# Kernel optimization log

Hardware: AMD Instinct MI355X
Metric: run time of the kernel (lower is better)

## Reference

```python
import jax, jax.numpy as jnp
import numpy as np

TIME_STEPS = 50
LEFT_PAD = 250 // TIME_STEPS            # 5
MAX_DELAY = LEFT_PAD if LEFT_PAD % 2 == 1 else LEFT_PAD + 1  # 5 (odd)
SIG = float(MAX_DELAY // 2)             # 2.0, frozen
CIN = 34 * 34 * 2                       # 2312
HID = 300
NOUT = 10
BETA = 0.9
THRESH = 1.0
BATCH = 128


def setup_inputs() -> dict:
    key = jax.random.key(0)
    k = jax.random.split(key, 6)
    data = jax.random.normal(k[0], (BATCH, TIME_STEPS, CIN), jnp.float32)
    W1 = jax.random.normal(k[1], (HID, CIN), jnp.float32) / np.sqrt(CIN * MAX_DELAY).astype(np.float32)
    P1 = jax.random.uniform(k[2], (HID, CIN), jnp.float32, -SIG, SIG)
    b1 = jnp.zeros((HID,), jnp.float32)
    W2 = jax.random.normal(k[3], (NOUT, HID), jnp.float32) / np.sqrt(HID * MAX_DELAY).astype(np.float32)
    P2 = jax.random.uniform(k[4], (NOUT, HID), jnp.float32, -SIG, SIG)
    b2 = jnp.zeros((NOUT,), jnp.float32)
    return {"data": data, "W1": W1, "P1": P1, "b1": b1, "W2": W2, "P2": P2, "b2": b2}


def make_gauss_kernel(W, P):
    # DCLS 'gauss': weight W placed at learnable position P (centered at KS//2)
    # with Gaussian of width SIG, normalized over the KS taps. kernel_count=1.
    idx = jnp.arange(MAX_DELAY, dtype=W.dtype)              # [KS]
    c = P[..., None] + (MAX_DELAY // 2)                     # [O, I, 1]
    g = jnp.exp(-0.5 * ((idx - c) / SIG) ** 2)              # [O, I, KS]
    g = g / (g.sum(-1, keepdims=True) + 1e-7)
    return W[..., None] * g                                 # [O, I, KS]


def delay_conv(x, W, P, b):
    # x: [B, Cin, L], valid conv with synthesized kernel -> [B, Cout, L-KS+1]
    K = make_gauss_kernel(W, P)
    y = jax.lax.conv_general_dilated(x, K, window_strides=(1,), padding='VALID',
                                     dimension_numbers=('NCH', 'OIH', 'NCH'))
    return y + b[None, :, None]


def lif_scan(x):
    # snntorch Leaky (reset-by-subtraction, reset detached):
    #   mem_t = beta*mem_{t-1} + x_t - H(mem_{t-1}-thr)*thr ;  spk_t = H(mem_t-thr)
    # x: [B, C, T] -> (spk [T,B,C], mem [T,B,C])
    def step(mem, xt):
        reset = (mem > THRESH).astype(xt.dtype)
        mem_new = BETA * mem + xt - reset * THRESH
        spk = (mem_new > THRESH).astype(xt.dtype)
        return mem_new, (spk, mem_new)

    xs = jnp.moveaxis(x, 2, 0)                              # [T, B, C]
    mem0 = jnp.zeros(x.shape[:2], x.dtype)
    _, (spks, mems) = jax.lax.scan(step, mem0, xs)
    return spks, mems


def reference(data, W1, P1, b1, W2, P2, b2):
    # pad time (dim -2) on the left, permute to [B, Cin, T+pad]
    x = jnp.pad(data, ((0, 0), (LEFT_PAD, 0), (0, 0)))
    x = jnp.transpose(x, (0, 2, 1))                         # [B, CIN, T+pad]
    x = delay_conv(x, W1, P1, b1)                           # [B, HID, T1]
    spk1, _ = lif_scan(x)                                   # [T1, B, HID]
    h = jnp.moveaxis(spk1, 0, 2)                            # [B, HID, T1]
    h = jnp.pad(h, ((0, 0), (0, 0), (LEFT_PAD, 0)))
    y = delay_conv(h, W2, P2, b2)                           # [B, NOUT, T2]
    spk2, mem2 = lif_scan(y)                                # [T2, B, NOUT] each
    return spk2, mem2
```

## Files before the change

### kernel.cpp

```cpp
#include <hip/hip_runtime.h>

#define BSZ  128
#define TT   50
#define CIN  2312
#define HID  300
#define NOUT 10
#define KS   5
#define T1   51
#define T2   52

#define NC32 73
#define KFRAG_U 20480

typedef unsigned int u32;
typedef unsigned short u16;
typedef __attribute__((ext_vector_type(8))) short s16x8;
typedef __attribute__((ext_vector_type(4))) float f32x4;

#define EK1f 0.88249690258459546f
#define EK2f 0.60653065971263342f
#define EK3f 0.32465246735834974f
#define EK4f 0.13533528323661270f

static __device__ __forceinline__ u16 bfhi(float x) {
  u32 u = __float_as_uint(x);
  return (u16)((u + 0x7fffu + ((u >> 16) & 1u)) >> 16);
}
static __device__ __forceinline__ float bf2f(u16 h) {
  return __uint_as_float(((u32)h) << 16);
}

__global__ __launch_bounds__(256) void snn_prepm(
    const float* __restrict__ W1, const float* __restrict__ P1,
    u16* __restrict__ K1bf)
{
  const int c  = blockIdx.x;
  const int ow = blockIdx.y;
  const int tid = threadIdx.x;
  const int nt = tid >> 6, ll = tid & 63;
  const int g = ll >> 4, lr = ll & 15;
  const int o  = ow * 64 + nt * 16 + lr;
  const int ib = c * 32 + g * 8;

  s16x8 hv[5], lv[5];
#pragma unroll
  for (int k = 0; k < 5; ++k)
#pragma unroll
    for (int j = 0; j < 8; ++j) { hv[k][j] = 0; lv[k][j] = 0; }

  if (o < HID) {
    const float* wrow = W1 + (size_t)o * CIN;
    const float* prow = P1 + (size_t)o * CIN;
#pragma unroll
    for (int j = 0; j < 8; ++j) {
      const int i = ib + j;
      if (i < CIN) {
        const float w1 = wrow[i], p1 = prow[i];
        const float cc = p1 + 2.0f;
        const float E0 = __expf(-0.125f * cc * cc);
        const float U  = __expf(0.25f * cc);
        const float u2 = U * U;
        const float e0 = E0;
        const float e1 = E0 * U * EK1f;
        const float e2 = E0 * u2 * EK2f;
        const float e3 = E0 * (u2 * U) * EK3f;
        const float e4 = E0 * (u2 * u2) * EK4f;
        const float inv = 1.0f / (((((e0 + e1) + e2) + e3) + e4) + 1e-7f);
        const float vk[5] = { w1 * (e0 * inv), w1 * (e1 * inv),
                              w1 * (e2 * inv), w1 * (e3 * inv),
                              w1 * (e4 * inv) };
#pragma unroll
        for (int k = 0; k < 5; ++k) {
          const u16 h = bfhi(vk[k]);
          const u16 lo = bfhi(vk[k] - bf2f(h));
          hv[k][j] = (short)h; lv[k][j] = (short)lo;
        }
      }
    }
  }
  u16* base = K1bf + ((size_t)ow * NC32 + c) * KFRAG_U + nt * 1024 + ll * 8;
#pragma unroll
  for (int k = 0; k < 5; ++k) {
    *(s16x8*)(base + k * 4096)       = hv[k];
    *(s16x8*)(base + k * 4096 + 512) = lv[k];
  }
}

__global__ __launch_bounds__(256, 2) void snn_l1s(
    const float* __restrict__ data, const u16* __restrict__ K1bf,
    float* __restrict__ pbuf)
{
  __shared__ __align__(16) double dsm[2720];
  u16* A16 = (u16*)dsm;

  const int tid = threadIdx.x;
  const int bid = blockIdx.x;
  const int g  = bid & 7;
  const int r  = bid >> 3;
  const int s  = r & 1;
  const int u  = r >> 1;
  const int x  = g * 80 + u;
  const int ow = x >> 7;
  const int b  = x & 127;

  const int c_lo = s ? 37 : 0;
  const int c_hi = s ? 73 : 37;

  const int w  = tid >> 6, l = tid & 63;
  const int lr = l & 15, lg = l >> 4;
  const int wr = w >> 1, wc = w & 1;
  const int abase_u = (32 * wr + lr) * 40 + lg * 8;

  const float* dbase = data + (size_t)b * (TT * CIN);
  const u16* kbn = K1bf + (size_t)ow * NC32 * KFRAG_U + l * 8;
  const int ntg0 = wc * 2, ntg1 = wc * 2 + 1;

  const int s1 = tid >> 2;
  const int j4 = tid & 3;
  const int tp = s1 - 5;
  const bool avld = (tp >= 0) && (tp < TT);
  const float* aptr = dbase + (size_t)(avld ? tp : 0) * CIN + j4 * 8;

  if (tid < 80) {
    s16x8 z;
#pragma unroll
    for (int j = 0; j < 8; ++j) z[j] = 0;
    const int rr = tid / 20, off = (tid % 20) * 8;
    *(s16x8*)(A16 + rr * 2720 + 2560 + off) = z;
  }

#define LOADA(CC)                                                             \
  {                                                                           \
    const bool iv_ = avld && (((CC) < 72) || (j4 == 0));                      \
    const float* pp_ = aptr + (size_t)(CC) * 32;                              \
    ra0 = iv_ ? *(const float4*)(pp_)     : make_float4(0.f, 0.f, 0.f, 0.f);  \
    ra1 = iv_ ? *(const float4*)(pp_ + 4) : make_float4(0.f, 0.f, 0.f, 0.f);  \
  }

#define STAGE_A(CC)                                                           \
  {                                                                           \
    const float f_[8] = { ra0.x, ra0.y, ra0.z, ra0.w,                         \
                          ra1.x, ra1.y, ra1.z, ra1.w };                       \
    s16x8 hv_, lv_;                                                           \
    _Pragma("unroll")                                                         \
    for (int j = 0; j < 8; ++j) {                                             \
      const u16 h_ = bfhi(f_[j]);                                             \
      hv_[j] = (short)h_;                                                     \
      lv_[j] = (short)bfhi(f_[j] - bf2f(h_));                                 \
    }                                                                         \
    u16* bn_ = A16 + ((CC) & 1) * 5440;                                       \
    const int woff_ = s1 * 40 + j4 * 8;                                       \
    *(s16x8*)(bn_ + woff_) = hv_;                                             \
    *(s16x8*)(bn_ + 2720 + woff_) = lv_;                                      \
  }

  s16x8 bh[5][2], bl[5][2];
#pragma unroll
  for (int k = 0; k < 5; ++k) {
    const u16* cb_ = kbn + (size_t)c_lo * KFRAG_U + k * 4096;
    bh[k][0] = *(const s16x8*)(cb_ + ntg0 * 1024);
    bh[k][1] = *(const s16x8*)(cb_ + ntg1 * 1024);
    bl[k][0] = *(const s16x8*)(cb_ + ntg0 * 1024 + 512);
    bl[k][1] = *(const s16x8*)(cb_ + ntg1 * 1024 + 512);
  }

  f32x4 accf[2][2];
  double accd[2][2][4];
#pragma unroll
  for (int m = 0; m < 2; ++m)
#pragma unroll
    for (int n = 0; n < 2; ++n)
#pragma unroll
      for (int q = 0; q < 4; ++q) { accf[m][n][q] = 0.f; accd[m][n][q] = 0.0; }

  float4 ra0, ra1;
  LOADA(c_lo);
  STAGE_A(c_lo);
  LOADA(c_lo + 1);
  __syncthreads();

  for (int c = c_lo; c < c_hi; ++c) {
    if (c + 1 < c_hi) {
      STAGE_A(c + 1);
      if (c + 2 < c_hi) LOADA(c + 2);
    }

    {
      const u16* bc_ = A16 + (c & 1) * 5440;
      const int rc = c + 1;
#pragma unroll
      for (int k = 0; k < 5; ++k) {
        const s16x8 ah0 = *(const s16x8*)(bc_ + abase_u + k * 40);
        const s16x8 al0 = *(const s16x8*)(bc_ + 2720 + abase_u + k * 40);
        const s16x8 ah1 = *(const s16x8*)(bc_ + abase_u + (16 + k) * 40);
        const s16x8 al1 = *(const s16x8*)(bc_ + 2720 + abase_u + (16 + k) * 40);

        accf[0][0] = __builtin_amdgcn_mfma_f32_16x16x32_bf16(ah0, bh[k][0], accf[0][0], 0, 0, 0);
        accf[0][0] = __builtin_amdgcn_mfma_f32_16x16x32_bf16(al0, bh[k][0], accf[0][0], 0, 0, 0);
        accf[0][0] = __builtin_amdgcn_mfma_f32_16x16x32_bf16(ah0, bl[k][0], accf[0][0], 0, 0, 0);

        accf[0][1] = __builtin_amdgcn_mfma_f32_16x16x32_bf16(ah0, bh[k][1], accf[0][1], 0, 0, 0);
        accf[0][1] = __builtin_amdgcn_mfma_f32_16x16x32_bf16(al0, bh[k][1], accf[0][1], 0, 0, 0);
        accf[0][1] = __builtin_amdgcn_mfma_f32_16x16x32_bf16(ah0, bl[k][1], accf[0][1], 0, 0, 0);

        accf[1][0] = __builtin_amdgcn_mfma_f32_16x16x32_bf16(ah1, bh[k][0], accf[1][0], 0, 0, 0);
        accf[1][0] = __builtin_amdgcn_mfma_f32_16x16x32_bf16(al1, bh[k][0], accf[1][0], 0, 0, 0);
        accf[1][0] = __builtin_amdgcn_mfma_f32_16x16x32_bf16(ah1, bl[k][0], accf[1][0], 0, 0, 0);

        accf[1][1] = __builtin_amdgcn_mfma_f32_16x16x32_bf16(ah1, bh[k][1], accf[1][1], 0, 0, 0);
        accf[1][1] = __builtin_amdgcn_mfma_f32_16x16x32_bf16(al1, bh[k][1], accf[1][1], 0, 0, 0);
        accf[1][1] = __builtin_amdgcn_mfma_f32_16x16x32_bf16(ah1, bl[k][1], accf[1][1], 0, 0, 0);

        if (rc < c_hi) {
          const u16* cb_ = kbn + (size_t)rc * KFRAG_U + k * 4096;
          bh[k][0] = *(const s16x8*)(cb_ + ntg0 * 1024);
          bh[k][1] = *(const s16x8*)(cb_ + ntg1 * 1024);
          bl[k][0] = *(const s16x8*)(cb_ + ntg0 * 1024 + 512);
          bl[k][1] = *(const s16x8*)(cb_ + ntg1 * 1024 + 512);
        }
      }
    }

#pragma unroll
    for (int m = 0; m < 2; ++m)
#pragma unroll
      for (int n = 0; n < 2; ++n)
#pragma unroll
        for (int q = 0; q < 4; ++q) {
          accd[m][n][q] += (double)accf[m][n][q];
          accf[m][n][q] = 0.f;
        }
    __syncthreads();
  }
#undef LOADA
#undef STAGE_A

  float* pb = pbuf + (((size_t)s * 5 + ow) * 128 + b) * 3264;
#pragma unroll
  for (int m = 0; m < 2; ++m)
#pragma unroll
    for (int n = 0; n < 2; ++n)
#pragma unroll
      for (int q = 0; q < 4; ++q) {
        const int t = 32 * wr + 16 * m + lg * 4 + q;
        if (t < T1) pb[t * 64 + 32 * wc + 16 * n + lr] = (float)accd[m][n][q];
      }
}

__global__ __launch_bounds__(256) void snn_l2m(
    const float* __restrict__ pbuf, const float* __restrict__ b1v,
    const float* __restrict__ W2, const float* __restrict__ P2,
    const float* __restrict__ b2, float* __restrict__ out)
{
  __shared__ float smem[16030];
  const int b = blockIdx.x, tid = threadIdx.x;
  float* K2s = smem;
  u32* lbits = (u32*)(smem + 15000);
  float* y2s = smem + 15510;

  for (int idx = tid; idx < NOUT * HID; idx += 256) {
    const int o = idx / HID, i = idx % HID;
    const float w = W2[idx], p = P2[idx];
    const float c = p + 2.0f;
    float e[KS], ssum = 0.f;
#pragma unroll
    for (int k = 0; k < KS; ++k) {
      const float d = ((float)k - c) * 0.5f;
      e[k] = __expf(-0.5f * d * d);
      ssum += e[k];
    }
    const float denom = ssum + 1e-7f;
#pragma unroll
    for (int k = 0; k < KS; ++k)
      K2s[(o * KS + k) * HID + i] = w * (e[k] / denom);
  }

  {
    const int w = tid >> 6, l = tid & 63;
    for (int ow = w; ow < 5; ow += 4) {
      const int o = ow * 64 + l;
      const bool valid = o < HID;
      const double bias = valid ? (double)b1v[o] : 0.0;
      const float* p0 = pbuf + (((size_t)0 * 5 + ow) * 128 + b) * 3264 + l;
      const float* p1 = pbuf + (((size_t)1 * 5 + ow) * 128 + b) * 3264 + l;
      double mem = 0.0;
      for (int t = 0; t < T1; ++t) {
        const double x = (double)p0[t * 64] + (double)p1[t * 64] + bias;
        const double reset = (mem > 1.0) ? 1.0 : 0.0;
        mem = __dsub_rn(__dadd_rn(__dmul_rn(0.9, mem), x), reset);
        const unsigned long long mk = __ballot(valid && (mem > 1.0));
        if (l == 0)  lbits[t * 10 + 2 * ow]     = (u32)mk;
        if (l == 32) lbits[t * 10 + 2 * ow + 1] = (u32)(mk >> 32);
      }
    }
  }
  __syncthreads();

  for (int task = tid; task < T2 * NOUT; task += 256) {
    const int t2 = task / NOUT, o = task % NOUT;
    float acc = b2[o];
#pragma unroll
    for (int k = 0; k < KS; ++k) {
      const int tp = t2 + k - KS;
      if (tp < 0 || tp >= T1) continue;
      const float* kr = K2s + (o * KS + k) * HID;
      const u32* br = lbits + tp * 10;
      for (int i = 0; i < HID; ++i)
        acc = fmaf((float)((br[i >> 5] >> (i & 31)) & 1u), kr[i], acc);
    }
    y2s[task] = acc;
  }
  __syncthreads();

  if (tid < NOUT) {
    float mem = 0.f;
    for (int t = 0; t < T2; ++t) {
      const float x = y2s[t * NOUT + tid];
      const float reset = (mem > 1.0f) ? 1.0f : 0.0f;
      mem = __fsub_rn(__fadd_rn(__fmul_rn(0.9f, mem), x), reset);
      out[(size_t)t * (BSZ * NOUT) + b * NOUT + tid] = (mem > 1.0f) ? 1.0f : 0.0f;
      out[(size_t)T2 * BSZ * NOUT + (size_t)t * (BSZ * NOUT) + b * NOUT + tid] = mem;
    }
  }
}

__global__ __launch_bounds__(256, 2) void snn_l1m(
    const float* __restrict__ data, const u16* __restrict__ K1bf,
    const float* __restrict__ b1v, u32* __restrict__ gbits)
{
  __shared__ double dsm[3264];
  u16* A16 = (u16*)dsm;

  const int tid = threadIdx.x;
  const int bid = blockIdx.x;
  const int rnk = (bid & 7) * 80 + (bid >> 3);
  const int ow = rnk >> 7;
  const int b  = rnk & 127;

  const int w  = tid >> 6, l = tid & 63;
  const int lr = l & 15, lg = l >> 4;
  const int wr = w >> 1, wc = w & 1;
  const int abase_u = (32 * wr + lr) * 40 + lg * 8;

  const float* dbase = data + (size_t)b * (TT * CIN);
  const u16* kbn = K1bf + (size_t)ow * NC32 * KFRAG_U + l * 8;
  const int ntg0 = wc * 2, ntg1 = wc * 2 + 1;

  const int s1 = tid >> 2;
  const int j4 = tid & 3;
  const int tp = s1 - 5;
  const bool avld = (tp >= 0) && (tp < TT);
  const float* aptr = dbase + (size_t)(avld ? tp : 0) * CIN + j4 * 8;

  if (tid < 80) {
    s16x8 z;
#pragma unroll
    for (int j = 0; j < 8; ++j) z[j] = 0;
    const int rr = tid / 20, off = (tid % 20) * 8;
    *(s16x8*)(A16 + rr * 2720 + 2560 + off) = z;
  }

#define LOADA(CC)                                                             \
  {                                                                           \
    const bool iv_ = avld && (((CC) < 72) || (j4 == 0));                      \
    const float* pp_ = aptr + (size_t)(CC) * 32;                              \
    ra0 = iv_ ? *(const float4*)(pp_)     : make_float4(0.f, 0.f, 0.f, 0.f);  \
    ra1 = iv_ ? *(const float4*)(pp_ + 4) : make_float4(0.f, 0.f, 0.f, 0.f);  \
  }

#define STAGE_A(CC)                                                           \
  {                                                                           \
    const float f_[8] = { ra0.x, ra0.y, ra0.z, ra0.w,                         \
                          ra1.x, ra1.y, ra1.z, ra1.w };                       \
    s16x8 hv_, lv_;                                                           \
    _Pragma("unroll")                                                         \
    for (int j = 0; j < 8; ++j) {                                             \
      const u16 h_ = bfhi(f_[j]);                                             \
      hv_[j] = (short)h_;                                                     \
      lv_[j] = (short)bfhi(f_[j] - bf2f(h_));                                 \
    }                                                                         \
    u16* bn_ = A16 + ((CC) & 1) * 5440;                                       \
    const int woff_ = s1 * 40 + j4 * 8;                                       \
    *(s16x8*)(bn_ + woff_) = hv_;                                             \
    *(s16x8*)(bn_ + 2720 + woff_) = lv_;                                      \
  }

  s16x8 bh[5][2], bl[5][2];
#pragma unroll
  for (int k = 0; k < 5; ++k) {
    const u16* cb_ = kbn + k * 4096;
    bh[k][0] = *(const s16x8*)(cb_ + ntg0 * 1024);
    bh[k][1] = *(const s16x8*)(cb_ + ntg1 * 1024);
    bl[k][0] = *(const s16x8*)(cb_ + ntg0 * 1024 + 512);
    bl[k][1] = *(const s16x8*)(cb_ + ntg1 * 1024 + 512);
  }

  f32x4 accf[2][2];
  double accd[2][2][4];
#pragma unroll
  for (int m = 0; m < 2; ++m)
#pragma unroll
    for (int n = 0; n < 2; ++n)
#pragma unroll
      for (int q = 0; q < 4; ++q) { accf[m][n][q] = 0.f; accd[m][n][q] = 0.0; }

  float4 ra0, ra1;
  LOADA(0);
  STAGE_A(0);
  LOADA(1);
  __syncthreads();

  for (int c = 0; c < NC32; ++c) {
    if (c + 1 < NC32) {
      STAGE_A(c + 1);
      if (c + 2 < NC32) LOADA(c + 2);
    }
    {
      const u16* bc_ = A16 + (c & 1) * 5440;
      const int rc = c + 1;
#pragma unroll
      for (int k = 0; k < 5; ++k) {
        const s16x8 ah0 = *(const s16x8*)(bc_ + abase_u + k * 40);
        const s16x8 al0 = *(const s16x8*)(bc_ + 2720 + abase_u + k * 40);
        const s16x8 ah1 = *(const s16x8*)(bc_ + abase_u + (16 + k) * 40);
        const s16x8 al1 = *(const s16x8*)(bc_ + 2720 + abase_u + (16 + k) * 40);

        accf[0][0] = __builtin_amdgcn_mfma_f32_16x16x32_bf16(ah0, bh[k][0], accf[0][0], 0, 0, 0);
        accf[0][0] = __builtin_amdgcn_mfma_f32_16x16x32_bf16(al0, bh[k][0], accf[0][0], 0, 0, 0);
        accf[0][0] = __builtin_amdgcn_mfma_f32_16x16x32_bf16(ah0, bl[k][0], accf[0][0], 0, 0, 0);
        accf[0][1] = __builtin_amdgcn_mfma_f32_16x16x32_bf16(ah0, bh[k][1], accf[0][1], 0, 0, 0);
        accf[0][1] = __builtin_amdgcn_mfma_f32_16x16x32_bf16(al0, bh[k][1], accf[0][1], 0, 0, 0);
        accf[0][1] = __builtin_amdgcn_mfma_f32_16x16x32_bf16(ah0, bl[k][1], accf[0][1], 0, 0, 0);
        accf[1][0] = __builtin_amdgcn_mfma_f32_16x16x32_bf16(ah1, bh[k][0], accf[1][0], 0, 0, 0);
        accf[1][0] = __builtin_amdgcn_mfma_f32_16x16x32_bf16(al1, bh[k][0], accf[1][0], 0, 0, 0);
        accf[1][0] = __builtin_amdgcn_mfma_f32_16x16x32_bf16(ah1, bl[k][0], accf[1][0], 0, 0, 0);
        accf[1][1] = __builtin_amdgcn_mfma_f32_16x16x32_bf16(ah1, bh[k][1], accf[1][1], 0, 0, 0);
        accf[1][1] = __builtin_amdgcn_mfma_f32_16x16x32_bf16(al1, bh[k][1], accf[1][1], 0, 0, 0);
        accf[1][1] = __builtin_amdgcn_mfma_f32_16x16x32_bf16(ah1, bl[k][1], accf[1][1], 0, 0, 0);

        if (rc < NC32) {
          const u16* cb_ = kbn + (size_t)rc * KFRAG_U + k * 4096;
          bh[k][0] = *(const s16x8*)(cb_ + ntg0 * 1024);
          bh[k][1] = *(const s16x8*)(cb_ + ntg1 * 1024);
          bl[k][0] = *(const s16x8*)(cb_ + ntg0 * 1024 + 512);
          bl[k][1] = *(const s16x8*)(cb_ + ntg1 * 1024 + 512);
        }
      }
    }
#pragma unroll
    for (int m = 0; m < 2; ++m)
#pragma unroll
      for (int n = 0; n < 2; ++n)
#pragma unroll
        for (int q = 0; q < 4; ++q) {
          accd[m][n][q] += (double)accf[m][n][q];
          accf[m][n][q] = 0.f;
        }
    __syncthreads();
  }
#undef LOADA
#undef STAGE_A

  double* y1s = dsm;
#pragma unroll
  for (int m = 0; m < 2; ++m)
#pragma unroll
    for (int n = 0; n < 2; ++n)
#pragma unroll
      for (int q = 0; q < 4; ++q) {
        const int t = 32 * wr + 16 * m + lg * 4 + q;
        if (t < T1) y1s[t * 64 + 32 * wc + 16 * n + lr] = accd[m][n][q];
      }
  __syncthreads();

  if (tid < 64) {
    const int o = ow * 64 + tid;
    const bool valid = o < HID;
    const double bias = valid ? (double)b1v[o] : 0.0;
    u32* bits = gbits + (size_t)b * 510;
    double mem = 0.0;
    for (int t = 0; t < T1; ++t) {
      const double x = y1s[t * 64 + tid] + bias;
      const double reset = (mem > 1.0) ? 1.0 : 0.0;
      mem = __dsub_rn(__dadd_rn(__dmul_rn(0.9, mem), x), reset);
      const unsigned long long mk = __ballot(valid && (mem > 1.0));
      if (tid == 0)  bits[t * 10 + 2 * ow]     = (u32)mk;
      if (tid == 32) bits[t * 10 + 2 * ow + 1] = (u32)(mk >> 32);
    }
  }
}

__device__ __forceinline__ void layer1_tile_g(
    int b, int ow, int tid,
    const float* __restrict__ data, const float* __restrict__ W1,
    const float* __restrict__ P1, const float* __restrict__ b1v,
    double* __restrict__ dsm, u32* __restrict__ bits)
{
  float* Bsf = (float*)dsm;
  float* As  = (float*)dsm + 2880;

  const int ty = tid >> 5;
  const int tx = tid & 31;
  const int r0 = ty << 3;
  const int c0 = tx << 1;

  const float* abase = data + (size_t)b * (TT * CIN);

  const int slot = tid >> 2;
  const int pair = tid & 3;
  const int tp   = slot - 5;

  const int isub = tid & 7;
  const int oA = tid >> 3;
  const int oB = oA + 32;
  const int boA = ow * 64 + oA;
  const int boB = ow * 64 + oB;
  const bool vB = boB < HID;

  double acc[8][2];
#pragma unroll
  for (int r = 0; r < 8; ++r) { acc[r][0] = 0.0; acc[r][1] = 0.0; }

  float2 aA = make_float2(0.f, 0.f);
  float wA = 0.f, pA = 0.f, wB = 0.f, pB = 0.f;
  if (tid < 220 && tp >= 0)
    aA = *(const float2*)(abase + (size_t)tp * CIN + 2 * pair);
  wA = W1[(size_t)boA * CIN + isub];
  pA = P1[(size_t)boA * CIN + isub];
  if (vB) {
    wB = W1[(size_t)boB * CIN + isub];
    pB = P1[(size_t)boB * CIN + isub];
  }

  for (int i0 = 0; i0 < CIN; i0 += 8) {
    if (tid < 220) {
      As[(2 * pair) * 80 + slot]     = aA.x;
      As[(2 * pair + 1) * 80 + slot] = aA.y;
    }
    {
      const float c  = pA + 2.0f;
      const float E0 = __expf(-0.125f * c * c);
      const float U  = __expf(0.25f * c);
      const float u2 = U * U;
      const float e0 = E0;
      const float e1 = E0 * U * EK1f;
      const float e2 = E0 * u2 * EK2f;
      const float e3 = E0 * (u2 * U) * EK3f;
      const float e4 = E0 * (u2 * u2) * EK4f;
      const float inv = 1.0f / (((((e0 + e1) + e2) + e3) + e4) + 1e-7f);
      float* bp = Bsf + isub * 72 + oA;
      bp[0]    = wA * (e0 * inv);
      bp[576]  = wA * (e1 * inv);
      bp[1152] = wA * (e2 * inv);
      bp[1728] = wA * (e3 * inv);
      bp[2304] = wA * (e4 * inv);
    }
    {
      const float c  = pB + 2.0f;
      const float E0 = __expf(-0.125f * c * c);
      const float U  = __expf(0.25f * c);
      const float u2 = U * U;
      const float e0 = E0;
      const float e1 = E0 * U * EK1f;
      const float e2 = E0 * u2 * EK2f;
      const float e3 = E0 * (u2 * U) * EK3f;
      const float e4 = E0 * (u2 * u2) * EK4f;
      const float inv = 1.0f / (((((e0 + e1) + e2) + e3) + e4) + 1e-7f);
      float* bp = Bsf + isub * 72 + oB;
      bp[0]    = wB * (e0 * inv);
      bp[576]  = wB * (e1 * inv);
      bp[1152] = wB * (e2 * inv);
      bp[1728] = wB * (e3 * inv);
      bp[2304] = wB * (e4 * inv);
    }
    __syncthreads();

    const int i0n = i0 + 8;
    if (i0n < CIN) {
      if (tid < 220 && tp >= 0)
        aA = *(const float2*)(abase + (size_t)tp * CIN + i0n + 2 * pair);
      wA = W1[(size_t)boA * CIN + i0n + isub];
      pA = P1[(size_t)boA * CIN + i0n + isub];
      if (vB) {
        wB = W1[(size_t)boB * CIN + i0n + isub];
        pB = P1[(size_t)boB * CIN + i0n + isub];
      }
    }

    float accf[8][2];
#pragma unroll
    for (int r = 0; r < 8; ++r) { accf[r][0] = 0.f; accf[r][1] = 0.f; }
#pragma unroll
    for (int kk = 0; kk < 8; ++kk) {
      const float* ap = &As[kk * 80 + r0];
      const float4 a0 = *(const float4*)(ap);
      const float4 a1 = *(const float4*)(ap + 4);
      const float4 a2 = *(const float4*)(ap + 8);
      float av[12];
      av[0] = a0.x; av[1] = a0.y; av[2]  = a0.z; av[3]  = a0.w;
      av[4] = a1.x; av[5] = a1.y; av[6]  = a1.z; av[7]  = a1.w;
      av[8] = a2.x; av[9] = a2.y; av[10] = a2.z; av[11] = a2.w;
      float bv[KS][2];
#pragma unroll
      for (int k = 0; k < KS; ++k) {
        const float2 bb = *(const float2*)&Bsf[(k * 8 + kk) * 72 + c0];
        bv[k][0] = bb.x; bv[k][1] = bb.y;
      }
#pragma unroll
      for (int k = 0; k < KS; ++k)
#pragma unroll
        for (int r = 0; r < 8; ++r) {
          accf[r][0] = fmaf(av[r + k], bv[k][0], accf[r][0]);
          accf[r][1] = fmaf(av[r + k], bv[k][1], accf[r][1]);
        }
    }
#pragma unroll
    for (int r = 0; r < 8; ++r) {
      acc[r][0] += (double)accf[r][0];
      acc[r][1] += (double)accf[r][1];
    }
    __syncthreads();
  }

  double* y1s = dsm;
#pragma unroll
  for (int r = 0; r < 8; ++r) {
    const int t = r0 + r;
    if (t < T1) {
      y1s[t * 64 + c0]     = acc[r][0];
      y1s[t * 64 + c0 + 1] = acc[r][1];
    }
  }
  __syncthreads();

  if (tid < 64) {
    const int o = ow * 64 + tid;
    const bool valid = o < HID;
    const double bias = valid ? (double)b1v[o] : 0.0;
    double mem = 0.0;
    for (int t = 0; t < T1; ++t) {
      const double x = y1s[t * 64 + tid] + bias;
      const double reset = (mem > 1.0) ? 1.0 : 0.0;
      mem = __dsub_rn(__dadd_rn(__dmul_rn(0.9, mem), x), reset);
      const unsigned long long mk = __ballot(valid && (mem > 1.0));
      if (tid == 0)  bits[t * 10 + 2 * ow]     = (u32)mk;
      if (tid == 32) bits[t * 10 + 2 * ow + 1] = (u32)(mk >> 32);
    }
  }
  __syncthreads();
}

__device__ __forceinline__ void layer2_lif2(
    int b, int tid, float* smem,
    const float* __restrict__ W2, const float* __restrict__ P2,
    const float* __restrict__ b2, float* __restrict__ out)
{
  float* K2s = smem;
  const u32* lbits = (const u32*)(smem + 15000);
  float* y2s = smem + 15510;

  for (int idx = tid; idx < NOUT * HID; idx += 256) {
    const int o = idx / HID, i = idx % HID;
    const float w = W2[idx], p = P2[idx];
    const float c = p + 2.0f;
    float e[KS], s = 0.f;
#pragma unroll
    for (int k = 0; k < KS; ++k) {
      const float d = ((float)k - c) * 0.5f;
      e[k] = __expf(-0.5f * d * d);
      s += e[k];
    }
    const float denom = s + 1e-7f;
#pragma unroll
    for (int k = 0; k < KS; ++k)
      K2s[(o * KS + k) * HID + i] = w * (e[k] / denom);
  }
  __syncthreads();

  for (int task = tid; task < T2 * NOUT; task += 256) {
    const int t2 = task / NOUT, o = task % NOUT;
    float acc = b2[o];
#pragma unroll
    for (int k = 0; k < KS; ++k) {
      const int tp = t2 + k - KS;
      if (tp < 0 || tp >= T1) continue;
      const float* kr = K2s + (o * KS + k) * HID;
      const u32* br = lbits + tp * 10;
      for (int i = 0; i < HID; ++i)
        acc = fmaf((float)((br[i >> 5] >> (i & 31)) & 1u), kr[i], acc);
    }
    y2s[task] = acc;
  }
  __syncthreads();

  if (tid < NOUT) {
    float mem = 0.f;
    for (int t = 0; t < T2; ++t) {
      const float x = y2s[t * NOUT + tid];
      const float reset = (mem > 1.0f) ? 1.0f : 0.0f;
      mem = __fsub_rn(__fadd_rn(__fmul_rn(0.9f, mem), x), reset);
      out[(size_t)t * (BSZ * NOUT) + b * NOUT + tid] = (mem > 1.0f) ? 1.0f : 0.0f;
      out[(size_t)T2 * BSZ * NOUT + (size_t)t * (BSZ * NOUT) + b * NOUT + tid] = mem;
    }
  }
}

__global__ __launch_bounds__(256) void snn_l1(
    const float* __restrict__ data, const float* __restrict__ W1,
    const float* __restrict__ P1, const float* __restrict__ b1v,
    u32* __restrict__ gbits)
{
  __shared__ double dsm[3264];
  const int ow = blockIdx.x, b = blockIdx.y;
  layer1_tile_g(b, ow, threadIdx.x, data, W1, P1, b1v, dsm,
                gbits + (size_t)b * 510);
}

__global__ __launch_bounds__(256) void snn_l2k(
    const u32* __restrict__ gbits,
    const float* __restrict__ W2, const float* __restrict__ P2,
    const float* __restrict__ b2, float* __restrict__ out)
{
  __shared__ float smem[16030];
  const int b = blockIdx.x, tid = threadIdx.x;
  u32* lbits = (u32*)(smem + 15000);
  for (int i = tid; i < 510; i += 256) lbits[i] = gbits[(size_t)b * 510 + i];
  layer2_lif2(b, tid, smem, W2, P2, b2, out);
}

__global__ __launch_bounds__(256) void snn_mono(
    const float* __restrict__ data, const float* __restrict__ W1,
    const float* __restrict__ P1, const float* __restrict__ b1v,
    const float* __restrict__ W2, const float* __restrict__ P2,
    const float* __restrict__ b2, float* __restrict__ out)
{
  __shared__ double dsm[8015];
  const int b = blockIdx.x, tid = threadIdx.x;
  u32* lbits = (u32*)((float*)dsm + 15000);
  for (int ow = 0; ow < 5; ++ow)
    layer1_tile_g(b, ow, tid, data, W1, P1, b1v, dsm, lbits);
  layer2_lif2(b, tid, (float*)dsm, W2, P2, b2, out);
}

extern "C" void kernel_launch(void* const* d_in, const int* in_sizes, int n_in,
                              void* d_out, int out_size, void* d_ws, size_t ws_size,
                              hipStream_t stream) {
  const float* data = (const float*)d_in[0];
  const float* W1   = (const float*)d_in[1];
  const float* P1   = (const float*)d_in[2];
  const float* b1v  = (const float*)d_in[3];
  const float* W2   = (const float*)d_in[4];
  const float* P2   = (const float*)d_in[5];
  const float* b2   = (const float*)d_in[6];
  float* out = (float*)d_out;

  const size_t BITS_BYTES  = (size_t)BSZ * T1 * 10 * sizeof(u32);
  const size_t K1BF_BYTES  = (size_t)5 * NC32 * KFRAG_U * 2;
  const size_t PBUF_BYTES  = (size_t)2 * 5 * 128 * 3264 * 4;
  const size_t NEED_S = PBUF_BYTES + K1BF_BYTES;
  const size_t K1_OFF_M = 262144;
  const size_t NEED_M = K1_OFF_M + K1BF_BYTES;

  if (ws_size >= NEED_S) {
    float* pbuf = (float*)d_ws;
    u16* K1bf   = (u16*)((char*)d_ws + PBUF_BYTES);
    snn_prepm<<<dim3(NC32, 5), 256, 0, stream>>>(W1, P1, K1bf);
    snn_l1s<<<1280, 256, 0, stream>>>(data, K1bf, pbuf);
    snn_l2m<<<BSZ, 256, 0, stream>>>(pbuf, b1v, W2, P2, b2, out);
  } else if (ws_size >= NEED_M) {
    u32* gbits = (u32*)d_ws;
    u16* K1bf  = (u16*)((char*)d_ws + K1_OFF_M);
    snn_prepm<<<dim3(NC32, 5), 256, 0, stream>>>(W1, P1, K1bf);
    snn_l1m<<<640, 256, 0, stream>>>(data, K1bf, b1v, gbits);
    snn_l2k<<<BSZ, 256, 0, stream>>>(gbits, W2, P2, b2, out);
  } else if (ws_size >= BITS_BYTES) {
    u32* gbits = (u32*)d_ws;
    snn_l1<<<dim3(5, BSZ), 256, 0, stream>>>(data, W1, P1, b1v, gbits);
    snn_l2k<<<BSZ, 256, 0, stream>>>(gbits, W2, P2, b2, out);
  } else {
    snn_mono<<<BSZ, 256, 0, stream>>>(data, W1, P1, b1v, W2, P2, b2, out);
  }
}
```

Baseline: 410.8 us.

## Process two batch rows per block to reuse kernel fragments and drop double accumulation

```diff
diff --git a/kernel.cpp b/kernel.cpp
--- a/kernel.cpp
+++ b/kernel.cpp
@@ -90,90 +90,98 @@
     const float* __restrict__ data, const u16* __restrict__ K1bf,
     float* __restrict__ pbuf)
 {
-  __shared__ __align__(16) double dsm[2720];
-  u16* A16 = (u16*)dsm;
+  __shared__ __align__(16) u16 A16[21760];
 
   const int tid = threadIdx.x;
   const int bid = blockIdx.x;
   const int g  = bid & 7;
-  const int r  = bid >> 3;
-  const int s  = r & 1;
-  const int u  = r >> 1;
+  const int u  = bid >> 3;
   const int x  = g * 80 + u;
   const int ow = x >> 7;
-  const int b  = x & 127;
+  const int rem = x & 127;
+  const int s  = rem >> 6;
+  const int bp = rem & 63;
+  const int b0 = 2 * bp;
 
   const int c_lo = s ? 37 : 0;
   const int c_hi = s ? 73 : 37;
 
   const int w  = tid >> 6, l = tid & 63;
   const int lr = l & 15, lg = l >> 4;
-  const int wr = w >> 1, wc = w & 1;
-  const int abase_u = (32 * wr + lr) * 40 + lg * 8;
-
-  const float* dbase = data + (size_t)b * (TT * CIN);
+  const int wb = w >> 1, wc = w & 1;
+  const int ntg0 = wc * 2, ntg1 = wc * 2 + 1;
+
   const u16* kbn = K1bf + (size_t)ow * NC32 * KFRAG_U + l * 8;
-  const int ntg0 = wc * 2, ntg1 = wc * 2 + 1;
 
   const int s1 = tid >> 2;
   const int j4 = tid & 3;
   const int tp = s1 - 5;
   const bool avld = (tp >= 0) && (tp < TT);
-  const float* aptr = dbase + (size_t)(avld ? tp : 0) * CIN + j4 * 8;
-
-  if (tid < 80) {
+  const float* aptrA = data + (size_t)b0 * (TT * CIN)
+                       + (size_t)(avld ? tp : 0) * CIN + j4 * 8;
+  const float* aptrB = aptrA + (size_t)(TT * CIN);
+
+  if (tid < 160) {
     s16x8 z;
 #pragma unroll
     for (int j = 0; j < 8; ++j) z[j] = 0;
-    const int rr = tid / 20, off = (tid % 20) * 8;
-    *(s16x8*)(A16 + rr * 2720 + 2560 + off) = z;
+    const int r = tid / 20, off = (tid % 20) * 8;
+    *(s16x8*)(A16 + (r >> 2) * 10880 + ((r >> 1) & 1) * 5440
+              + (r & 1) * 2720 + 2560 + off) = z;
   }
 
 #define LOADA(CC)                                                             \
   {                                                                           \
     const bool iv_ = avld && (((CC) < 72) || (j4 == 0));                      \
-    const float* pp_ = aptr + (size_t)(CC) * 32;                              \
-    ra0 = iv_ ? *(const float4*)(pp_)     : make_float4(0.f, 0.f, 0.f, 0.f);  \
-    ra1 = iv_ ? *(const float4*)(pp_ + 4) : make_float4(0.f, 0.f, 0.f, 0.f);  \
+    const float* pa_ = aptrA + (size_t)(CC) * 32;                             \
+    const float* pb_ = aptrB + (size_t)(CC) * 32;                             \
+    raA0 = iv_ ? *(const float4*)(pa_)     : make_float4(0.f, 0.f, 0.f, 0.f); \
+    raA1 = iv_ ? *(const float4*)(pa_ + 4) : make_float4(0.f, 0.f, 0.f, 0.f); \
+    raB0 = iv_ ? *(const float4*)(pb_)     : make_float4(0.f, 0.f, 0.f, 0.f); \
+    raB1 = iv_ ? *(const float4*)(pb_ + 4) : make_float4(0.f, 0.f, 0.f, 0.f); \
   }
 
 #define STAGE_A(CC)                                                           \
   {                                                                           \
-    const float f_[8] = { ra0.x, ra0.y, ra0.z, ra0.w,                         \
-                          ra1.x, ra1.y, ra1.z, ra1.w };                       \
-    s16x8 hv_, lv_;                                                           \
-    _Pragma("unroll")                                                         \
-    for (int j = 0; j < 8; ++j) {                                             \
-      const u16 h_ = bfhi(f_[j]);                                             \
-      hv_[j] = (short)h_;                                                     \
-      lv_[j] = (short)bfhi(f_[j] - bf2f(h_));                                 \
+    u16* bn_ = A16 + ((CC) & 1) * 10880;                                      \
+    const int woff_ = s1 * 40 + j4 * 8;                                       \
+    {                                                                         \
+      const float f_[8] = { raA0.x, raA0.y, raA0.z, raA0.w,                   \
+                            raA1.x, raA1.y, raA1.z, raA1.w };                 \
+      s16x8 hv_, lv_;                                                         \
+      _Pragma("unroll")                                                       \
+      for (int j = 0; j < 8; ++j) {                                           \
+        const u16 h_ = bfhi(f_[j]);                                           \
+        hv_[j] = (short)h_;                                                   \
+        lv_[j] = (short)bfhi(f_[j] - bf2f(h_));                               \
+      }                                                                       \
+      *(s16x8*)(bn_ + woff_) = hv_;                                           \
+      *(s16x8*)(bn_ + 2720 + woff_) = lv_;                                    \
     }                                                                         \
-    u16* bn_ = A16 + ((CC) & 1) * 5440;                                       \
-    const int woff_ = s1 * 40 + j4 * 8;                                       \
-    *(s16x8*)(bn_ + woff_) = hv_;                                             \
-    *(s16x8*)(bn_ + 2720 + woff_) = lv_;                                      \
-  }
-
-  s16x8 bh[5][2], bl[5][2];
-#pragma unroll
-  for (int k = 0; k < 5; ++k) {
-    const u16* cb_ = kbn + (size_t)c_lo * KFRAG_U + k * 4096;
-    bh[k][0] = *(const s16x8*)(cb_ + ntg0 * 1024);
-    bh[k][1] = *(const s16x8*)(cb_ + ntg1 * 1024);
-    bl[k][0] = *(const s16x8*)(cb_ + ntg0 * 1024 + 512);
-    bl[k][1] = *(const s16x8*)(cb_ + ntg1 * 1024 + 512);
-  }
-
-  f32x4 accf[2][2];
-  double accd[2][2][4];
-#pragma unroll
-  for (int m = 0; m < 2; ++m)
+    {                                                                         \
+      const float f_[8] = { raB0.x, raB0.y, raB0.z, raB0.w,                   \
+                            raB1.x, raB1.y, raB1.z, raB1.w };                 \
+      s16x8 hv_, lv_;                                                         \
+      _Pragma("unroll")                                                       \
+      for (int j = 0; j < 8; ++j) {                                           \
+        const u16 h_ = bfhi(f_[j]);                                           \
+        hv_[j] = (short)h_;                                                   \
+        lv_[j] = (short)bfhi(f_[j] - bf2f(h_));                               \
+      }                                                                       \
+      *(s16x8*)(bn_ + 5440 + woff_) = hv_;                                    \
+      *(s16x8*)(bn_ + 5440 + 2720 + woff_) = lv_;                             \
+    }                                                                         \
+  }
+
+  f32x4 accf[4][2];
+#pragma unroll
+  for (int m = 0; m < 4; ++m)
 #pragma unroll
     for (int n = 0; n < 2; ++n)
 #pragma unroll
-      for (int q = 0; q < 4; ++q) { accf[m][n][q] = 0.f; accd[m][n][q] = 0.0; }
-
-  float4 ra0, ra1;
+      for (int q = 0; q < 4; ++q) accf[m][n][q] = 0.f;
+
+  float4 raA0, raA1, raB0, raB1;
   LOADA(c_lo);
   STAGE_A(c_lo);
   LOADA(c_lo + 1);
@@ -186,64 +194,43 @@
     }
 
     {
-      const u16* bc_ = A16 + (c & 1) * 5440;
-      const int rc = c + 1;
+      const u16* cb_ = kbn + (size_t)c * KFRAG_U;
+      const u16* aw_ = A16 + (c & 1) * 10880 + wb * 5440;
 #pragma unroll
       for (int k = 0; k < 5; ++k) {
-        const s16x8 ah0 = *(const s16x8*)(bc_ + abase_u + k * 40);
-        const s16x8 al0 = *(const s16x8*)(bc_ + 2720 + abase_u + k * 40);
-        const s16x8 ah1 = *(const s16x8*)(bc_ + abase_u + (16 + k) * 40);
-        const s16x8 al1 = *(const s16x8*)(bc_ + 2720 + abase_u + (16 + k) * 40);
-
-        accf[0][0] = __builtin_amdgcn_mfma_f32_16x16x32_bf16(ah0, bh[k][0], accf[0][0], 0, 0, 0);
-        accf[0][0] = __builtin_amdgcn_mfma_f32_16x16x32_bf16(al0, bh[k][0], accf[0][0], 0, 0, 0);
-        accf[0][0] = __builtin_amdgcn_mfma_f32_16x16x32_bf16(ah0, bl[k][0], accf[0][0], 0, 0, 0);
-
-        accf[0][1] = __builtin_amdgcn_mfma_f32_16x16x32_bf16(ah0, bh[k][1], accf[0][1], 0, 0, 0);
-        accf[0][1] = __builtin_amdgcn_mfma_f32_16x16x32_bf16(al0, bh[k][1], accf[0][1], 0, 0, 0);
-        accf[0][1] = __builtin_amdgcn_mfma_f32_16x16x32_bf16(ah0, bl[k][1], accf[0][1], 0, 0, 0);
-
-        accf[1][0] = __builtin_amdgcn_mfma_f32_16x16x32_bf16(ah1, bh[k][0], accf[1][0], 0, 0, 0);
-        accf[1][0] = __builtin_amdgcn_mfma_f32_16x16x32_bf16(al1, bh[k][0], accf[1][0], 0, 0, 0);
-        accf[1][0] = __builtin_amdgcn_mfma_f32_16x16x32_bf16(ah1, bl[k][0], accf[1][0], 0, 0, 0);
-
-        accf[1][1] = __builtin_amdgcn_mfma_f32_16x16x32_bf16(ah1, bh[k][1], accf[1][1], 0, 0, 0);
-        accf[1][1] = __builtin_amdgcn_mfma_f32_16x16x32_bf16(al1, bh[k][1], accf[1][1], 0, 0, 0);
-        accf[1][1] = __builtin_amdgcn_mfma_f32_16x16x32_bf16(ah1, bl[k][1], accf[1][1], 0, 0, 0);
-
-        if (rc < c_hi) {
-          const u16* cb_ = kbn + (size_t)rc * KFRAG_U + k * 4096;
-          bh[k][0] = *(const s16x8*)(cb_ + ntg0 * 1024);
-          bh[k][1] = *(const s16x8*)(cb_ + ntg1 * 1024);
-          bl[k][0] = *(const s16x8*)(cb_ + ntg0 * 1024 + 512);
-          bl[k][1] = *(const s16x8*)(cb_ + ntg1 * 1024 + 512);
+        const u16* tb_ = cb_ + k * 4096;
+        const s16x8 bh0 = *(const s16x8*)(tb_ + ntg0 * 1024);
+        const s16x8 bl0 = *(const s16x8*)(tb_ + ntg0 * 1024 + 512);
+        const s16x8 bh1 = *(const s16x8*)(tb_ + ntg1 * 1024);
+        const s16x8 bl1 = *(const s16x8*)(tb_ + ntg1 * 1024 + 512);
+#pragma unroll
+        for (int m = 0; m < 4; ++m) {
+          const int ar_ = (16 * m + lr + k) * 40 + lg * 8;
+          const s16x8 ah = *(const s16x8*)(aw_ + ar_);
+          const s16x8 al = *(const s16x8*)(aw_ + 2720 + ar_);
+          accf[m][0] = __builtin_amdgcn_mfma_f32_16x16x32_bf16(ah, bh0, accf[m][0], 0, 0, 0);
+          accf[m][0] = __builtin_amdgcn_mfma_f32_16x16x32_bf16(al, bh0, accf[m][0], 0, 0, 0);
+          accf[m][0] = __builtin_amdgcn_mfma_f32_16x16x32_bf16(ah, bl0, accf[m][0], 0, 0, 0);
+          accf[m][1] = __builtin_amdgcn_mfma_f32_16x16x32_bf16(ah, bh1, accf[m][1], 0, 0, 0);
+          accf[m][1] = __builtin_amdgcn_mfma_f32_16x16x32_bf16(al, bh1, accf[m][1], 0, 0, 0);
+          accf[m][1] = __builtin_amdgcn_mfma_f32_16x16x32_bf16(ah, bl1, accf[m][1], 0, 0, 0);
         }
       }
     }
-
-#pragma unroll
-    for (int m = 0; m < 2; ++m)
-#pragma unroll
-      for (int n = 0; n < 2; ++n)
-#pragma unroll
-        for (int q = 0; q < 4; ++q) {
-          accd[m][n][q] += (double)accf[m][n][q];
-          accf[m][n][q] = 0.f;
-        }
     __syncthreads();
   }
 #undef LOADA
 #undef STAGE_A
 
-  float* pb = pbuf + (((size_t)s * 5 + ow) * 128 + b) * 3264;
-#pragma unroll
-  for (int m = 0; m < 2; ++m)
+  float* pb = pbuf + (((size_t)s * 5 + ow) * 128 + (b0 + wb)) * 3264;
+#pragma unroll
+  for (int m = 0; m < 4; ++m)
 #pragma unroll
     for (int n = 0; n < 2; ++n)
 #pragma unroll
       for (int q = 0; q < 4; ++q) {
-        const int t = 32 * wr + 16 * m + lg * 4 + q;
-        if (t < T1) pb[t * 64 + 32 * wc + 16 * n + lr] = (float)accd[m][n][q];
+        const int t = 16 * m + lg * 4 + q;
+        if (t < T1) pb[t * 64 + wc * 32 + n * 16 + lr] = accf[m][n][q];
       }
 }
 
@@ -765,7 +752,7 @@
     float* pbuf = (float*)d_ws;
     u16* K1bf   = (u16*)((char*)d_ws + PBUF_BYTES);
     snn_prepm<<<dim3(NC32, 5), 256, 0, stream>>>(W1, P1, K1bf);
-    snn_l1s<<<1280, 256, 0, stream>>>(data, K1bf, pbuf);
+    snn_l1s<<<640, 256, 0, stream>>>(data, K1bf, pbuf);
     snn_l2m<<<BSZ, 256, 0, stream>>>(pbuf, b1v, W2, P2, b2, out);
   } else if (ws_size >= NEED_M) {
     u32* gbits = (u32*)d_ws;
```

Result: faster. 392.3 us (-4.5%).
